# Performance work log

Measured on AMD Instinct MI355X. Metric: run time of the kernel, lower is better.

## Reference

```python
import jax, jax.numpy as jnp
import numpy as np
import jax.lax as lax

EPS_VAR = 1e-05  # hardcoded in original _get_statistics sqrt(var + 1e-05)


def _get_statistics(x):
    # x: (B, P, L). Cumulative NaN-aware mean/std along patch dim P.
    B, P, L = x.shape
    nan_mask = jnp.isnan(x)
    nan_counts = jnp.cumsum(nan_mask.sum(-1, keepdims=True).astype(x.dtype), axis=1)  # (B,P,1)
    counts = (jnp.arange(1, P + 1, dtype=x.dtype).reshape(1, P, 1)) * L - nan_counts   # (B,P,1)
    x0 = jnp.where(nan_mask, jnp.zeros_like(x), x)
    cumsum_x = jnp.cumsum(x0.sum(-1, keepdims=True), axis=1)          # nansum then cumsum
    mean = cumsum_x / counts
    cumsum_x2 = jnp.cumsum((x0 * x0).sum(-1, keepdims=True), axis=1)  # nansum of x^2
    var = (cumsum_x2 - 2.0 * mean * cumsum_x + counts * mean * mean) / counts
    std = jnp.sqrt(var + EPS_VAR)
    return mean, std


def _fill_nan_with_last_observed(x):
    # x: (B, P, L); forward-fill NaNs along last axis per (b,p) row.
    L = x.shape[-1]
    valid_mask = ~jnp.isnan(x)
    x_temp = jnp.where(valid_mask, x, jnp.zeros_like(x))
    seq_idx = jnp.arange(L, dtype=jnp.int32)
    valid_idx = jnp.where(valid_mask, seq_idx, jnp.int32(-1))
    last_valid = lax.cummax(valid_idx, axis=x.ndim - 1)
    return jnp.take_along_axis(x_temp, jnp.clip(last_valid, 0, None), axis=-1)


def setup_inputs() -> dict:
    key = jax.random.key(0)
    x = jax.random.normal(key, (128, 1024, 128), dtype=jnp.float32)
    return {"x": x}


def reference(x):
    # RevIN forward, mode='norm' (fresh cache). Original upcasts to float64;
    # we keep the input dtype (fp32) for kernel-comparison purposes.
    mean, std = _get_statistics(x)
    out = (x - mean) / std
    out = _fill_nan_with_last_observed(out)  # identity when no NaNs present
    return out.astype(jnp.float32)
```

## Files before the change

### kernel.cpp

```cpp
#include <hip/hip_runtime.h>
#include <math.h>

#define BB 128
#define PP 1024
#define LL 128
#define NROWS (BB * PP)
#define EPS_VAR 1e-5f

__device__ __forceinline__ bool is_nan_bits(float f) {
    return (__float_as_uint(f) & 0x7fffffffu) > 0x7f800000u;
}

__global__ __launch_bounds__(256) void k_rowstats(const float* __restrict__ x,
                                                  float4* __restrict__ stats) {
    const int wave = threadIdx.x >> 6;
    const int lane = threadIdx.x & 63;
    const int half = lane >> 5;
    const int sl   = lane & 31;
    const int row  = (blockIdx.x * 4 + wave) * 2 + half;

    const float4 v = ((const float4*)(x + (size_t)row * LL))[sl];

    float s1 = 0.f, s2 = 0.f, c = 0.f;
    {
        const float f[4] = {v.x, v.y, v.z, v.w};
#pragma unroll
        for (int j = 0; j < 4; ++j) {
            const bool nn = is_nan_bits(f[j]);
            const float vv = nn ? 0.f : f[j];
            s1 += vv;
            s2 += vv * vv;
            c  += nn ? 1.f : 0.f;
        }
    }
#pragma unroll
    for (int off = 16; off >= 1; off >>= 1) {
        s1 += __shfl_xor(s1, off);
        s2 += __shfl_xor(s2, off);
        c  += __shfl_xor(c,  off);
    }
    if (sl == 0) stats[row] = make_float4(s1, s2, c, 0.f);
}

__global__ __launch_bounds__(1024) void k_scan(const float4* __restrict__ stats,
                                               float2* __restrict__ ms) {
    __shared__ float a1[PP];
    __shared__ float a2[PP];
    __shared__ float ac[PP];

    const int t = threadIdx.x;
    const int b = blockIdx.x;

    const float4 s = stats[(size_t)b * PP + t];
    a1[t] = s.x; a2[t] = s.y; ac[t] = s.z;
    __syncthreads();

#pragma unroll
    for (int off = 1; off < PP; off <<= 1) {
        float v1 = 0.f, v2 = 0.f, vc = 0.f;
        if (t >= off) { v1 = a1[t - off]; v2 = a2[t - off]; vc = ac[t - off]; }
        __syncthreads();
        if (t >= off) { a1[t] += v1; a2[t] += v2; ac[t] += vc; }
        __syncthreads();
    }

    const float cnt  = (float)(t + 1) * (float)LL - ac[t];
    const float mean = a1[t] / cnt;
    const float var  = a2[t] / cnt - mean * mean;
    const float istd = 1.0f / sqrtf(var + EPS_VAR);
    ms[(size_t)b * PP + t] = make_float2(mean, istd);
}

__global__ __launch_bounds__(256) void k_norm(const float* __restrict__ x,
                                              const float2* __restrict__ ms,
                                              float* __restrict__ out) {
    const int wave = threadIdx.x >> 6;
    const int lane = threadIdx.x & 63;
    const int half = lane >> 5;
    const int sl   = lane & 31;
    const int row  = (blockIdx.x * 4 + wave) * 2 + half;
    const size_t base = (size_t)row * LL;

    const float4 v = ((const float4*)(x + base))[sl];
    const float2 m = ms[row];

    float4 y;
    y.x = (v.x - m.x) * m.y;
    y.y = (v.y - m.x) * m.y;
    y.z = (v.z - m.x) * m.y;
    y.w = (v.w - m.x) * m.y;

    const bool n0 = is_nan_bits(v.x), n1 = is_nan_bits(v.y);
    const bool n2 = is_nan_bits(v.z), n3 = is_nan_bits(v.w);
    const bool anynan = n0 | n1 | n2 | n3;

    if (__ballot(anynan) == 0ull) {
        ((float4*)(out + base))[sl] = y;
    } else {
        const float yy[4] = {y.x, y.y, y.z, y.w};
        const bool  nn[4] = {n0, n1, n2, n3};
#pragma unroll
        for (int j = 0; j < 4; ++j) {
            const int l = sl * 4 + j;
            if (!nn[j]) {
                out[base + l] = yy[j];
            } else {
                float res = 0.0f;
                for (int k = l - 1; k >= 0; --k) {
                    const float xv = x[base + k];
                    if (!is_nan_bits(xv)) { res = (xv - m.x) * m.y; break; }
                }
                out[base + l] = res;
            }
        }
    }
}

extern "C" void kernel_launch(void* const* d_in, const int* in_sizes, int n_in,
                              void* d_out, int out_size, void* d_ws, size_t ws_size,
                              hipStream_t stream) {
    const float* x = (const float*)d_in[0];
    float* out = (float*)d_out;

    float4* stats = (float4*)d_ws;
    float2* ms    = (float2*)((char*)d_ws + (size_t)NROWS * sizeof(float4));

    k_rowstats<<<NROWS / 8, 256, 0, stream>>>(x, stats);
    k_scan<<<BB, PP, 0, stream>>>(stats, ms);
    k_norm<<<NROWS / 8, 256, 0, stream>>>(x, ms, out);
}
```

Measured before the change: 123.8 us.

## Process two rows per half-wave, warp-shuffle scan, and nontemporal output stores

The row-stats and normalize kernels now have each half-wave handle two rows, which halves the grid and puts more loads in flight per thread. The scan kernel replaces the 1024-thread shared-memory Hillis-Steele scan with 256 threads. Each thread does a serial scan over 4 elements, then a wave shuffle scan and a small cross-wave combine, which removes many barriers. Output stores in the normalize kernel use nontemporal hints to reduce cache pollution, at the cost of fewer waves for latency hiding.

```diff
diff --git a/kernel.cpp b/kernel.cpp
--- a/kernel.cpp
+++ b/kernel.cpp
@@ -7,110 +7,168 @@
 #define NROWS (BB * PP)
 #define EPS_VAR 1e-5f
 
+typedef float vfloat4 __attribute__((ext_vector_type(4)));
+
 __device__ __forceinline__ bool is_nan_bits(float f) {
     return (__float_as_uint(f) & 0x7fffffffu) > 0x7f800000u;
 }
 
 __global__ __launch_bounds__(256) void k_rowstats(const float* __restrict__ x,
                                                   float4* __restrict__ stats) {
-    const int wave = threadIdx.x >> 6;
-    const int lane = threadIdx.x & 63;
-    const int half = lane >> 5;
-    const int sl   = lane & 31;
-    const int row  = (blockIdx.x * 4 + wave) * 2 + half;
+    const int sl = threadIdx.x & 31;
+    const int hw = (blockIdx.x * 256 + threadIdx.x) >> 5;
+    const int row0 = hw * 2;
+    const int row1 = row0 + 1;
 
-    const float4 v = ((const float4*)(x + (size_t)row * LL))[sl];
+    const float4 v0 = ((const float4*)(x + (size_t)row0 * LL))[sl];
+    const float4 v1 = ((const float4*)(x + (size_t)row1 * LL))[sl];
 
-    float s1 = 0.f, s2 = 0.f, c = 0.f;
+    float s1a = 0.f, s2a = 0.f, ca = 0.f;
+    float s1b = 0.f, s2b = 0.f, cb = 0.f;
     {
-        const float f[4] = {v.x, v.y, v.z, v.w};
+        const float fa[4] = {v0.x, v0.y, v0.z, v0.w};
+        const float fb[4] = {v1.x, v1.y, v1.z, v1.w};
 #pragma unroll
         for (int j = 0; j < 4; ++j) {
-            const bool nn = is_nan_bits(f[j]);
-            const float vv = nn ? 0.f : f[j];
-            s1 += vv;
-            s2 += vv * vv;
-            c  += nn ? 1.f : 0.f;
+            const bool na = is_nan_bits(fa[j]);
+            const float va = na ? 0.f : fa[j];
+            s1a += va; s2a += va * va; ca += na ? 1.f : 0.f;
+            const bool nb = is_nan_bits(fb[j]);
+            const float vb = nb ? 0.f : fb[j];
+            s1b += vb; s2b += vb * vb; cb += nb ? 1.f : 0.f;
         }
     }
 #pragma unroll
     for (int off = 16; off >= 1; off >>= 1) {
-        s1 += __shfl_xor(s1, off);
-        s2 += __shfl_xor(s2, off);
-        c  += __shfl_xor(c,  off);
+        s1a += __shfl_xor(s1a, off);
+        s2a += __shfl_xor(s2a, off);
+        ca  += __shfl_xor(ca,  off);
+        s1b += __shfl_xor(s1b, off);
+        s2b += __shfl_xor(s2b, off);
+        cb  += __shfl_xor(cb,  off);
     }
-    if (sl == 0) stats[row] = make_float4(s1, s2, c, 0.f);
+    if (sl == 0) {
+        stats[row0] = make_float4(s1a, s2a, ca, 0.f);
+        stats[row1] = make_float4(s1b, s2b, cb, 0.f);
+    }
 }
 
-__global__ __launch_bounds__(1024) void k_scan(const float4* __restrict__ stats,
-                                               float2* __restrict__ ms) {
-    __shared__ float a1[PP];
-    __shared__ float a2[PP];
-    __shared__ float ac[PP];
+__global__ __launch_bounds__(256) void k_scan(const float4* __restrict__ stats,
+                                              float2* __restrict__ ms) {
+    __shared__ float w1[4], w2[4], wc[4];
 
-    const int t = threadIdx.x;
-    const int b = blockIdx.x;
+    const int t    = threadIdx.x;
+    const int lane = t & 63;
+    const int wav  = t >> 6;
+    const int b    = blockIdx.x;
+    const size_t base = (size_t)b * PP + t * 4;
 
-    const float4 s = stats[(size_t)b * PP + t];
-    a1[t] = s.x; a2[t] = s.y; ac[t] = s.z;
+    float4 r[4];
+#pragma unroll
+    for (int j = 0; j < 4; ++j) r[j] = stats[base + j];
+
+    float i1[4], i2[4], ic[4];
+    i1[0] = r[0].x; i2[0] = r[0].y; ic[0] = r[0].z;
+#pragma unroll
+    for (int j = 1; j < 4; ++j) {
+        i1[j] = i1[j - 1] + r[j].x;
+        i2[j] = i2[j - 1] + r[j].y;
+        ic[j] = ic[j - 1] + r[j].z;
+    }
+    const float t1 = i1[3], t2 = i2[3], tc = ic[3];
+
+    float c1 = t1, c2 = t2, cc = tc;
+#pragma unroll
+    for (int off = 1; off < 64; off <<= 1) {
+        const float a   = __shfl_up(c1, off);
+        const float bb2 = __shfl_up(c2, off);
+        const float cc2 = __shfl_up(cc, off);
+        if (lane >= off) { c1 += a; c2 += bb2; cc += cc2; }
+    }
+    const float e1 = c1 - t1, e2 = c2 - t2, ec = cc - tc;
+
+    if (lane == 63) { w1[wav] = c1; w2[wav] = c2; wc[wav] = cc; }
     __syncthreads();
 
+    float p1 = 0.f, p2 = 0.f, pc = 0.f;
 #pragma unroll
-    for (int off = 1; off < PP; off <<= 1) {
-        float v1 = 0.f, v2 = 0.f, vc = 0.f;
-        if (t >= off) { v1 = a1[t - off]; v2 = a2[t - off]; vc = ac[t - off]; }
-        __syncthreads();
-        if (t >= off) { a1[t] += v1; a2[t] += v2; ac[t] += vc; }
-        __syncthreads();
+    for (int k = 0; k < 3; ++k) {
+        if (wav > k) { p1 += w1[k]; p2 += w2[k]; pc += wc[k]; }
     }
 
-    const float cnt  = (float)(t + 1) * (float)LL - ac[t];
-    const float mean = a1[t] / cnt;
-    const float var  = a2[t] / cnt - mean * mean;
-    const float istd = 1.0f / sqrtf(var + EPS_VAR);
-    ms[(size_t)b * PP + t] = make_float2(mean, istd);
+    const float b1 = p1 + e1, b2 = p2 + e2, bc = pc + ec;
+    float2 o[4];
+#pragma unroll
+    for (int j = 0; j < 4; ++j) {
+        const int p = t * 4 + j;
+        const float cum1 = b1 + i1[j];
+        const float cum2 = b2 + i2[j];
+        const float cumc = bc + ic[j];
+        const float cnt  = (float)(p + 1) * (float)LL - cumc;
+        const float mean = cum1 / cnt;
+        const float var  = cum2 / cnt - mean * mean;
+        const float istd = 1.0f / sqrtf(var + EPS_VAR);
+        o[j] = make_float2(mean, istd);
+    }
+    float2* dst = ms + base;
+#pragma unroll
+    for (int j = 0; j < 4; ++j) dst[j] = o[j];
 }
 
 __global__ __launch_bounds__(256) void k_norm(const float* __restrict__ x,
                                               const float2* __restrict__ ms,
                                               float* __restrict__ out) {
-    const int wave = threadIdx.x >> 6;
-    const int lane = threadIdx.x & 63;
-    const int half = lane >> 5;
-    const int sl   = lane & 31;
-    const int row  = (blockIdx.x * 4 + wave) * 2 + half;
-    const size_t base = (size_t)row * LL;
+    const int sl = threadIdx.x & 31;
+    const int hw = (blockIdx.x * 256 + threadIdx.x) >> 5;
+    const int row0 = hw * 2;
+    const int row1 = row0 + 1;
+    const size_t base0 = (size_t)row0 * LL;
+    const size_t base1 = (size_t)row1 * LL;
 
-    const float4 v = ((const float4*)(x + base))[sl];
-    const float2 m = ms[row];
+    const float4 v0 = ((const float4*)(x + base0))[sl];
+    const float4 v1 = ((const float4*)(x + base1))[sl];
+    const float2 m0 = ms[row0];
+    const float2 m1 = ms[row1];
 
-    float4 y;
-    y.x = (v.x - m.x) * m.y;
-    y.y = (v.y - m.x) * m.y;
-    y.z = (v.z - m.x) * m.y;
-    y.w = (v.w - m.x) * m.y;
+    float4 y0, y1;
+    y0.x = (v0.x - m0.x) * m0.y; y0.y = (v0.y - m0.x) * m0.y;
+    y0.z = (v0.z - m0.x) * m0.y; y0.w = (v0.w - m0.x) * m0.y;
+    y1.x = (v1.x - m1.x) * m1.y; y1.y = (v1.y - m1.x) * m1.y;
+    y1.z = (v1.z - m1.x) * m1.y; y1.w = (v1.w - m1.x) * m1.y;
 
-    const bool n0 = is_nan_bits(v.x), n1 = is_nan_bits(v.y);
-    const bool n2 = is_nan_bits(v.z), n3 = is_nan_bits(v.w);
-    const bool anynan = n0 | n1 | n2 | n3;
+    const bool anynan = is_nan_bits(v0.x) | is_nan_bits(v0.y) | is_nan_bits(v0.z) |
+                        is_nan_bits(v0.w) | is_nan_bits(v1.x) | is_nan_bits(v1.y) |
+                        is_nan_bits(v1.z) | is_nan_bits(v1.w);
 
     if (__ballot(anynan) == 0ull) {
-        ((float4*)(out + base))[sl] = y;
+        vfloat4 w0 = {y0.x, y0.y, y0.z, y0.w};
+        vfloat4 w1 = {y1.x, y1.y, y1.z, y1.w};
+        __builtin_nontemporal_store(w0, &((vfloat4*)(out + base0))[sl]);
+        __builtin_nontemporal_store(w1, &((vfloat4*)(out + base1))[sl]);
     } else {
-        const float yy[4] = {y.x, y.y, y.z, y.w};
-        const bool  nn[4] = {n0, n1, n2, n3};
+        const size_t bases[2] = {base0, base1};
+        const float2 mm[2] = {m0, m1};
+        const float4 vv[2] = {v0, v1};
+        const float4 yy[2] = {y0, y1};
 #pragma unroll
-        for (int j = 0; j < 4; ++j) {
-            const int l = sl * 4 + j;
-            if (!nn[j]) {
-                out[base + l] = yy[j];
-            } else {
-                float res = 0.0f;
-                for (int k = l - 1; k >= 0; --k) {
-                    const float xv = x[base + k];
-                    if (!is_nan_bits(xv)) { res = (xv - m.x) * m.y; break; }
+        for (int rr = 0; rr < 2; ++rr) {
+            const float yf[4] = {yy[rr].x, yy[rr].y, yy[rr].z, yy[rr].w};
+            const float vf[4] = {vv[rr].x, vv[rr].y, vv[rr].z, vv[rr].w};
+            for (int j = 0; j < 4; ++j) {
+                const int l = sl * 4 + j;
+                if (!is_nan_bits(vf[j])) {
+                    out[bases[rr] + l] = yf[j];
+                } else {
+                    float res = 0.0f;
+                    for (int k = l - 1; k >= 0; --k) {
+                        const float xv = x[bases[rr] + k];
+                        if (!is_nan_bits(xv)) {
+                            res = (xv - mm[rr].x) * mm[rr].y;
+                            break;
+                        }
+                    }
+                    out[bases[rr] + l] = res;
                 }
-                out[base + l] = res;
             }
         }
     }
@@ -125,7 +183,7 @@
     float4* stats = (float4*)d_ws;
     float2* ms    = (float2*)((char*)d_ws + (size_t)NROWS * sizeof(float4));
 
-    k_rowstats<<<NROWS / 8, 256, 0, stream>>>(x, stats);
-    k_scan<<<BB, PP, 0, stream>>>(stats, ms);
-    k_norm<<<NROWS / 8, 256, 0, stream>>>(x, ms, out);
+    k_rowstats<<<NROWS / 16, 256, 0, stream>>>(x, stats);
+    k_scan<<<BB, 256, 0, stream>>>(stats, ms);
+    k_norm<<<NROWS / 16, 256, 0, stream>>>(x, ms, out);
 }
```

After: 120.6 us. 1.03x faster.

## Fuse row stats, scan and normalize into chunked two-kernel decoupled scan

Applied to the files above, without the earlier changes.

Replaces the three-kernel pipeline (per-row stats, per-batch 1024-thread scan, normalize) with two kernels. The first computes per-chunk totals over 128-row chunks. The second reloads its chunk into registers, recomputes row stats, does a local wave-shuffle scan, adds prefix offsets from the chunk totals, and writes normalized output with nontemporal stores. This removes the per-row stats and mean/std workspace round trips and the heavily synchronized shared-memory scan. In exchange, x is read twice, each thread keeps 16 float4 values in registers, and a serial prefix loop over the chunk totals runs in one thread.

```diff
diff --git a/kernel.cpp b/kernel.cpp
--- a/kernel.cpp
+++ b/kernel.cpp
@@ -6,112 +6,165 @@
 #define LL 128
 #define NROWS (BB * PP)
 #define EPS_VAR 1e-5f
+#define NBLK 1024
+#define ROWS_PER_BLK 128
+#define CHUNKS 8
+
+typedef float vfloat4 __attribute__((ext_vector_type(4)));
 
 __device__ __forceinline__ bool is_nan_bits(float f) {
     return (__float_as_uint(f) & 0x7fffffffu) > 0x7f800000u;
 }
 
-__global__ __launch_bounds__(256) void k_rowstats(const float* __restrict__ x,
-                                                  float4* __restrict__ stats) {
-    const int wave = threadIdx.x >> 6;
-    const int lane = threadIdx.x & 63;
-    const int half = lane >> 5;
-    const int sl   = lane & 31;
-    const int row  = (blockIdx.x * 4 + wave) * 2 + half;
+__global__ __launch_bounds__(256) void k_chunktot(const float* __restrict__ x,
+                                                  float4* __restrict__ tot) {
+    __shared__ float ws1[4], ws2[4], wsc[4];
+    const int g = blockIdx.x;
+    const int t = threadIdx.x;
+    const int lane = t & 63;
+    const int wav  = t >> 6;
 
-    const float4 v = ((const float4*)(x + (size_t)row * LL))[sl];
+    const vfloat4* px = (const vfloat4*)(x + (size_t)g * (ROWS_PER_BLK * LL));
 
     float s1 = 0.f, s2 = 0.f, c = 0.f;
-    {
-        const float f[4] = {v.x, v.y, v.z, v.w};
+#pragma unroll
+    for (int i = 0; i < 16; ++i) {
+        const vfloat4 v = px[t + 256 * i];
 #pragma unroll
         for (int j = 0; j < 4; ++j) {
-            const bool nn = is_nan_bits(f[j]);
-            const float vv = nn ? 0.f : f[j];
-            s1 += vv;
-            s2 += vv * vv;
-            c  += nn ? 1.f : 0.f;
+            const float f = v[j];
+            const bool nn = is_nan_bits(f);
+            const float u = nn ? 0.f : f;
+            s1 += u; s2 += u * u; c += nn ? 1.f : 0.f;
         }
     }
 #pragma unroll
-    for (int off = 16; off >= 1; off >>= 1) {
+    for (int off = 32; off >= 1; off >>= 1) {
         s1 += __shfl_xor(s1, off);
         s2 += __shfl_xor(s2, off);
         c  += __shfl_xor(c,  off);
     }
-    if (sl == 0) stats[row] = make_float4(s1, s2, c, 0.f);
+    if (lane == 0) { ws1[wav] = s1; ws2[wav] = s2; wsc[wav] = c; }
+    __syncthreads();
+    if (t == 0) {
+        tot[g] = make_float4(ws1[0] + ws1[1] + ws1[2] + ws1[3],
+                             ws2[0] + ws2[1] + ws2[2] + ws2[3],
+                             wsc[0] + wsc[1] + wsc[2] + wsc[3], 0.f);
+    }
 }
 
-__global__ __launch_bounds__(1024) void k_scan(const float4* __restrict__ stats,
-                                               float2* __restrict__ ms) {
-    __shared__ float a1[PP];
-    __shared__ float a2[PP];
-    __shared__ float ac[PP];
+__device__ __attribute__((noinline)) void slow_row(const float* __restrict__ x,
+                                                   float* __restrict__ out,
+                                                   size_t base, int sl,
+                                                   float mean, float istd,
+                                                   float4 vv) {
+    const float vf[4] = {vv.x, vv.y, vv.z, vv.w};
+    for (int j = 0; j < 4; ++j) {
+        const int l = sl * 4 + j;
+        if (!is_nan_bits(vf[j])) {
+            out[base + l] = (vf[j] - mean) * istd;
+        } else {
+            float res = 0.0f;
+            for (int k = l - 1; k >= 0; --k) {
+                const float xv = x[base + k];
+                if (!is_nan_bits(xv)) { res = (xv - mean) * istd; break; }
+            }
+            out[base + l] = res;
+        }
+    }
+}
 
-    const int t = threadIdx.x;
-    const int b = blockIdx.x;
+__global__ __launch_bounds__(256, 4) void k_scan_norm(const float* __restrict__ x,
+                                                      const float4* __restrict__ tot,
+                                                      float* __restrict__ out) {
+    __shared__ float ls1[ROWS_PER_BLK], ls2[ROWS_PER_BLK], lsc[ROWS_PER_BLK];
+    __shared__ float wtot[3];
+    __shared__ float off_s[3];
 
-    const float4 s = stats[(size_t)b * PP + t];
-    a1[t] = s.x; a2[t] = s.y; ac[t] = s.z;
+    const int g     = blockIdx.x;
+    const int b     = g >> 3;
+    const int chunk = g & 7;
+    const int t     = threadIdx.x;
+    const int sl    = t & 31;
+    const int h     = t >> 5;
+    const int p0    = chunk * ROWS_PER_BLK;
+    const size_t rowbase = (size_t)b * PP + p0;
+
+    float4 v[16];
+#pragma unroll
+    for (int i = 0; i < 16; ++i) {
+        const int r = h + 8 * i;
+        v[i] = ((const float4*)(x + (rowbase + r) * LL))[sl];
+    }
+#pragma unroll
+    for (int i = 0; i < 16; ++i) {
+        const int r = h + 8 * i;
+        const float f[4] = {v[i].x, v[i].y, v[i].z, v[i].w};
+        float s1 = 0.f, s2 = 0.f, c = 0.f;
+#pragma unroll
+        for (int j = 0; j < 4; ++j) {
+            const bool nn = is_nan_bits(f[j]);
+            const float u = nn ? 0.f : f[j];
+            s1 += u; s2 += u * u; c += nn ? 1.f : 0.f;
+        }
+#pragma unroll
+        for (int off = 16; off >= 1; off >>= 1) {
+            s1 += __shfl_xor(s1, off);
+            s2 += __shfl_xor(s2, off);
+            c  += __shfl_xor(c,  off);
+        }
+        if (sl == 0) { ls1[r] = s1; ls2[r] = s2; lsc[r] = c; }
+    }
     __syncthreads();
 
+    const int lane = t & 63;
+    float a1 = 0.f, a2 = 0.f, ac = 0.f;
+    if (t < 128) { a1 = ls1[t]; a2 = ls2[t]; ac = lsc[t]; }
 #pragma unroll
-    for (int off = 1; off < PP; off <<= 1) {
-        float v1 = 0.f, v2 = 0.f, vc = 0.f;
-        if (t >= off) { v1 = a1[t - off]; v2 = a2[t - off]; vc = ac[t - off]; }
-        __syncthreads();
-        if (t >= off) { a1[t] += v1; a2[t] += v2; ac[t] += vc; }
-        __syncthreads();
+    for (int off = 1; off < 64; off <<= 1) {
+        const float u1 = __shfl_up(a1, off);
+        const float u2 = __shfl_up(a2, off);
+        const float u3 = __shfl_up(ac, off);
+        if (lane >= off) { a1 += u1; a2 += u2; ac += u3; }
     }
+    if (t == 63) { wtot[0] = a1; wtot[1] = a2; wtot[2] = ac; }
+    __syncthreads();
+    if (t >= 64 && t < 128) { a1 += wtot[0]; a2 += wtot[1]; ac += wtot[2]; }
+    if (t < 128) { ls1[t] = a1; ls2[t] = a2; lsc[t] = ac; }
 
-    const float cnt  = (float)(t + 1) * (float)LL - ac[t];
-    const float mean = a1[t] / cnt;
-    const float var  = a2[t] / cnt - mean * mean;
-    const float istd = 1.0f / sqrtf(var + EPS_VAR);
-    ms[(size_t)b * PP + t] = make_float2(mean, istd);
-}
+    if (t == 0) {
+        float o1 = 0.f, o2 = 0.f, oc = 0.f;
+        for (int j = 0; j < chunk; ++j) {
+            const float4 ct = tot[(b << 3) + j];
+            o1 += ct.x; o2 += ct.y; oc += ct.z;
+        }
+        off_s[0] = o1; off_s[1] = o2; off_s[2] = oc;
+    }
+    __syncthreads();
+    const float o1 = off_s[0], o2 = off_s[1], oc = off_s[2];
 
-__global__ __launch_bounds__(256) void k_norm(const float* __restrict__ x,
-                                              const float2* __restrict__ ms,
-                                              float* __restrict__ out) {
-    const int wave = threadIdx.x >> 6;
-    const int lane = threadIdx.x & 63;
-    const int half = lane >> 5;
-    const int sl   = lane & 31;
-    const int row  = (blockIdx.x * 4 + wave) * 2 + half;
-    const size_t base = (size_t)row * LL;
+#pragma unroll
+    for (int i = 0; i < 16; ++i) {
+        const int r = h + 8 * i;
+        const float cum1 = o1 + ls1[r];
+        const float cum2 = o2 + ls2[r];
+        const float cumc = oc + lsc[r];
+        const int p = p0 + r;
+        const float cnt  = (float)((p + 1) * LL) - cumc;
+        const float mean = cum1 / cnt;
+        const float var  = cum2 / cnt - mean * mean;
+        const float istd = 1.0f / sqrtf(var + EPS_VAR);
+        const float4 vv = v[i];
+        const size_t base = (rowbase + r) * (size_t)LL;
 
-    const float4 v = ((const float4*)(x + base))[sl];
-    const float2 m = ms[row];
-
-    float4 y;
-    y.x = (v.x - m.x) * m.y;
-    y.y = (v.y - m.x) * m.y;
-    y.z = (v.z - m.x) * m.y;
-    y.w = (v.w - m.x) * m.y;
-
-    const bool n0 = is_nan_bits(v.x), n1 = is_nan_bits(v.y);
-    const bool n2 = is_nan_bits(v.z), n3 = is_nan_bits(v.w);
-    const bool anynan = n0 | n1 | n2 | n3;
-
-    if (__ballot(anynan) == 0ull) {
-        ((float4*)(out + base))[sl] = y;
-    } else {
-        const float yy[4] = {y.x, y.y, y.z, y.w};
-        const bool  nn[4] = {n0, n1, n2, n3};
-#pragma unroll
-        for (int j = 0; j < 4; ++j) {
-            const int l = sl * 4 + j;
-            if (!nn[j]) {
-                out[base + l] = yy[j];
-            } else {
-                float res = 0.0f;
-                for (int k = l - 1; k >= 0; --k) {
-                    const float xv = x[base + k];
-                    if (!is_nan_bits(xv)) { res = (xv - m.x) * m.y; break; }
-                }
-                out[base + l] = res;
-            }
+        const bool anynan = is_nan_bits(vv.x) | is_nan_bits(vv.y) |
+                            is_nan_bits(vv.z) | is_nan_bits(vv.w);
+        if (__ballot(anynan) == 0ull) {
+            vfloat4 y = {(vv.x - mean) * istd, (vv.y - mean) * istd,
+                         (vv.z - mean) * istd, (vv.w - mean) * istd};
+            __builtin_nontemporal_store(y, &((vfloat4*)(out + base))[sl]);
+        } else {
+            slow_row(x, out, base, sl, mean, istd, vv);
         }
     }
 }
@@ -120,12 +173,9 @@
                               void* d_out, int out_size, void* d_ws, size_t ws_size,
                               hipStream_t stream) {
     const float* x = (const float*)d_in[0];
-    float* out = (float*)d_out;
+    float* outp = (float*)d_out;
+    float4* tot = (float4*)d_ws;
 
-    float4* stats = (float4*)d_ws;
-    float2* ms    = (float2*)((char*)d_ws + (size_t)NROWS * sizeof(float4));
-
-    k_rowstats<<<NROWS / 8, 256, 0, stream>>>(x, stats);
-    k_scan<<<BB, PP, 0, stream>>>(stats, ms);
-    k_norm<<<NROWS / 8, 256, 0, stream>>>(x, ms, out);
+    k_chunktot<<<NBLK, 256, 0, stream>>>(x, tot);
+    k_scan_norm<<<NBLK, 256, 0, stream>>>(x, tot, outp);
 }
```

After: 135.2 us. 1.09x slower.
